# Performance work log

Measured on AMD Instinct MI355X. Metric: run time of the kernel, lower is better.

## Reference

```python
import jax, jax.numpy as jnp
import numpy as np

N_NODES = 50000
N_EDGES = 800000
N_FEAT = 32
DIM_ENC = 64
HEADS = 8
DIM_MLP = 512
NUM_GRAPHS = 2000
NEG_SLOPE = 0.2


def gat_conv(x, edge_index, W, a_src, a_dst, bias, concat):
    """PyG-style GATConv: add self loops, per-head attention, segment softmax over
    incoming edges at the destination node, weighted scatter-sum aggregation."""
    N = x.shape[0]
    H, F = a_src.shape
    h = (x @ W).reshape(N, H, F)                      # [N, H, F]
    loop = jnp.arange(N, dtype=edge_index.dtype)
    src = jnp.concatenate([edge_index[0], loop])      # source j
    dst = jnp.concatenate([edge_index[1], loop])      # target i
    alpha_src = (h * a_src[None]).sum(-1)             # [N, H]
    alpha_dst = (h * a_dst[None]).sum(-1)             # [N, H]
    e = alpha_src[src] + alpha_dst[dst]               # [E', H]
    e = jnp.where(e > 0, e, NEG_SLOPE * e)            # leaky_relu
    # segment softmax over edges sharing the same destination node
    m = jax.ops.segment_max(e, dst, num_segments=N)
    ex = jnp.exp(e - m[dst])
    s = jax.ops.segment_sum(ex, dst, num_segments=N)
    alpha = ex / (s[dst] + 1e-16)                     # [E', H]
    msg = h[src] * alpha[..., None]                   # [E', H, F]
    out = jax.ops.segment_sum(msg, dst, num_segments=N)  # [N, H, F]
    out = out.reshape(N, H * F) if concat else out.mean(axis=1)
    return out + bias


def setup_inputs() -> dict:
    key = jax.random.key(0)
    ks = jax.random.split(key, 16)
    x = jax.random.normal(ks[0], (N_NODES, N_FEAT), dtype=jnp.float32)
    edge_index = jax.random.randint(ks[1], (2, N_EDGES), 0, N_NODES, dtype=jnp.int64)
    batch = jnp.sort(jax.random.randint(ks[2], (N_NODES,), 0, NUM_GRAPHS, dtype=jnp.int64))
    sc = lambda fi, fo: 1.0 / np.sqrt(fi)
    W1 = jax.random.normal(ks[3], (N_FEAT, HEADS * DIM_ENC), dtype=jnp.float32) * sc(N_FEAT, 0)
    a_src1 = jax.random.normal(ks[4], (HEADS, DIM_ENC), dtype=jnp.float32) * sc(DIM_ENC, 0)
    a_dst1 = jax.random.normal(ks[5], (HEADS, DIM_ENC), dtype=jnp.float32) * sc(DIM_ENC, 0)
    b1 = jnp.zeros((DIM_ENC,), dtype=jnp.float32)
    W2 = jax.random.normal(ks[6], (DIM_ENC, HEADS * DIM_ENC), dtype=jnp.float32) * sc(DIM_ENC, 0)
    a_src2 = jax.random.normal(ks[7], (HEADS, DIM_ENC), dtype=jnp.float32) * sc(DIM_ENC, 0)
    a_dst2 = jax.random.normal(ks[8], (HEADS, DIM_ENC), dtype=jnp.float32) * sc(DIM_ENC, 0)
    b2 = jnp.zeros((HEADS * DIM_ENC,), dtype=jnp.float32)
    fcW1 = jax.random.normal(ks[9], (HEADS * DIM_ENC, DIM_MLP), dtype=jnp.float32) * sc(HEADS * DIM_ENC, 0)
    fcb1 = jnp.zeros((DIM_MLP,), dtype=jnp.float32)
    fcW2 = jax.random.normal(ks[10], (DIM_MLP, DIM_MLP), dtype=jnp.float32) * sc(DIM_MLP, 0)
    fcb2 = jnp.zeros((DIM_MLP,), dtype=jnp.float32)
    fcW3 = jax.random.normal(ks[11], (DIM_MLP, 1), dtype=jnp.float32) * sc(DIM_MLP, 0)
    fcb3 = jnp.zeros((1,), dtype=jnp.float32)
    return dict(x=x, edge_index=edge_index, batch=batch,
                W1=W1, a_src1=a_src1, a_dst1=a_dst1, b1=b1,
                W2=W2, a_src2=a_src2, a_dst2=a_dst2, b2=b2,
                fcW1=fcW1, fcb1=fcb1, fcW2=fcW2, fcb2=fcb2, fcW3=fcW3, fcb3=fcb3)


def reference(x, edge_index, batch, W1, a_src1, a_dst1, b1, W2, a_src2, a_dst2, b2,
              fcW1, fcb1, fcW2, fcb2, fcW3, fcb3):
    h = gat_conv(x, edge_index, W1, a_src1, a_dst1, b1, concat=False)   # [N, dim_enc]
    h = gat_conv(h, edge_index, W2, a_src2, a_dst2, b2, concat=True)    # [N, 8*dim_enc]
    g = jax.ops.segment_sum(h, batch, num_segments=NUM_GRAPHS)          # [G, 8*dim_enc]
    g = jax.nn.relu(g @ fcW1 + fcb1)   # dropout is identity in eval / p=0
    g = jax.nn.relu(g @ fcW2 + fcb2)
    return g @ fcW3 + fcb3             # [G, 1]
```

## Files before the change

kernel.cpp:

```cpp
#include <hip/hip_runtime.h>
#include <hip/hip_bf16.h>

#define N_NODES   50000
#define N_EDGES   800000
#define NF        32
#define DE        64
#define NH        8
#define CT        512
#define DMLP      512
#define NG        2000
#define NEGS      0.2f


__global__ void init_count_k(int* __restrict__ cnt) {
    int i = blockIdx.x * 256 + threadIdx.x;
    if (i < N_NODES) cnt[i] = 1;
}

__global__ void hist_k(const int* __restrict__ ei, int* __restrict__ cnt) {
    int e = blockIdx.x * 256 + threadIdx.x;
    if (e < N_EDGES) atomicAdd(&cnt[ei[N_EDGES + e]], 1);
}

__global__ void alloc_off_k(const int* __restrict__ cnt, int* __restrict__ off,
                            int* __restrict__ total) {
    int i = blockIdx.x * 256 + threadIdx.x;
    if (i < N_NODES) off[i] = atomicAdd(total, cnt[i]);
}

__global__ void scatter_k(const int* __restrict__ ei, const int* __restrict__ off,
                          int* __restrict__ cur, int* __restrict__ ssrc) {
    int e = blockIdx.x * 256 + threadIdx.x;
    if (e < N_EDGES) {
        int s = ei[e];
        int d = ei[N_EDGES + e];
        int p = off[d] + atomicAdd(&cur[d], 1);
        ssrc[p] = s;
    } else if (e < N_EDGES + N_NODES) {
        int i = e - N_EDGES;
        int p = off[i] + atomicAdd(&cur[i], 1);
        ssrc[p] = i;
    }
}


__global__ void goffs_k(const int* __restrict__ batch, int* __restrict__ goff) {
    int i = blockIdx.x * 256 + threadIdx.x;
    if (i >= N_NODES) return;
    int b = batch[i];
    if (i == 0) {
        for (int g = 0; g <= b; ++g) goff[g] = 0;
    } else {
        int pb = batch[i - 1];
        for (int g = pb + 1; g <= b; ++g) goff[g] = i;
    }
    if (i == N_NODES - 1) {
        for (int g = b + 1; g <= NG; ++g) goff[g] = N_NODES;
    }
}


__global__ void prep_k(const float* __restrict__ W1, const float* __restrict__ a_s1,
                       const float* __restrict__ a_d1, const float* __restrict__ W2,
                       const float* __restrict__ a_s2, const float* __restrict__ a_d2,
                       float* __restrict__ B1s, float* __restrict__ B1d,
                       float* __restrict__ B2s, float* __restrict__ B2d,
                       float* __restrict__ U1) {
    int idx = blockIdx.x * 256 + threadIdx.x;
    if (idx < 256) {
        int c = idx >> 3, hd = idx & 7;
        float s1 = 0.f, s2 = 0.f;
        for (int f = 0; f < 64; ++f) {
            float w = W1[c * 512 + hd * 64 + f];
            s1 += w * a_s1[hd * 64 + f];
            s2 += w * a_d1[hd * 64 + f];
        }
        B1s[idx] = s1; B1d[idx] = s2;
    } else if (idx < 768) {
        int i2 = idx - 256;
        int c = i2 >> 3, hd = i2 & 7;
        float s1 = 0.f, s2 = 0.f;
        for (int f = 0; f < 64; ++f) {
            float w = W2[c * 512 + hd * 64 + f];
            s1 += w * a_s2[hd * 64 + f];
            s2 += w * a_d2[hd * 64 + f];
        }
        B2s[i2] = s1; B2d[i2] = s2;
    } else if (idx < 768 + 256 * 64) {
        int i2 = idx - 768;
        int k = i2 >> 6, f = i2 & 63;
        int hd = k >> 5, c = k & 31;
        U1[i2] = W1[c * 512 + hd * 64 + f] * 0.125f;
    }
}


template<int C>
__global__ void alpha_x_k(const float* __restrict__ xin, const float* __restrict__ Bs,
                          const float* __restrict__ Bd, float* __restrict__ as_,
                          float* __restrict__ ad_) {
    __shared__ float bs[C * 8], bd[C * 8];
    int tid = threadIdx.x;
    for (int i = tid; i < C * 8; i += 256) { bs[i] = Bs[i]; bd[i] = Bd[i]; }
    __syncthreads();
    int gid = blockIdx.x * 256 + tid;
    if (gid >= N_NODES * NH) return;
    int n = gid >> 3, hd = gid & 7;
    const float4* xp = (const float4*)(xin + (size_t)n * C);
    float s1 = 0.f, s2 = 0.f;
    #pragma unroll
    for (int q = 0; q < C / 4; ++q) {
        float4 v = xp[q];
        int b0 = (q * 4) * 8 + hd;
        s1 += v.x * bs[b0] + v.y * bs[b0 + 8] + v.z * bs[b0 + 16] + v.w * bs[b0 + 24];
        s2 += v.x * bd[b0] + v.y * bd[b0 + 8] + v.z * bd[b0 + 16] + v.w * bd[b0 + 24];
    }
    as_[gid] = s1;
    ad_[gid] = s2;
}


__device__ inline float4 fma4(float a, float4 v, float4 c) {
    c.x = fmaf(a, v.x, c.x); c.y = fmaf(a, v.y, c.y);
    c.z = fmaf(a, v.z, c.z); c.w = fmaf(a, v.w, c.w);
    return c;
}

__device__ inline float edge_w(float e) {
    e = e > 0.f ? e : NEGS * e;
    return __expf(e);
}


__global__ __launch_bounds__(256) void agg1_k(
        const float* __restrict__ x, const float* __restrict__ as_,
        const float* __restrict__ ad_, const int* __restrict__ ssrc,
        const int* __restrict__ off, const int* __restrict__ cnt,
        float* __restrict__ aggx1) {
    int wv = __builtin_amdgcn_readfirstlane(blockIdx.x * 4 + (threadIdx.x >> 6));
    if (wv >= N_NODES) return;
    int lane = threadIdx.x & 63;
    int hd = lane >> 3, q = lane & 7;
    int beg = off[wv], end = beg + cnt[wv];
    float adv = ad_[wv * NH + hd];

    float4 acc = {0.f, 0.f, 0.f, 0.f};
    float wsum = 0.f;
    int j = beg;
    for (; j + 4 <= end; j += 4) {
        int s0 = ssrc[j], s1 = ssrc[j + 1], s2 = ssrc[j + 2], s3 = ssrc[j + 3];
        float e0 = as_[s0 * NH + hd], e1 = as_[s1 * NH + hd];
        float e2 = as_[s2 * NH + hd], e3 = as_[s3 * NH + hd];
        float4 v0 = *(const float4*)(x + s0 * NF + q * 4);
        float4 v1 = *(const float4*)(x + s1 * NF + q * 4);
        float4 v2 = *(const float4*)(x + s2 * NF + q * 4);
        float4 v3 = *(const float4*)(x + s3 * NF + q * 4);
        float w0 = edge_w(e0 + adv), w1 = edge_w(e1 + adv);
        float w2 = edge_w(e2 + adv), w3 = edge_w(e3 + adv);
        wsum += (w0 + w1) + (w2 + w3);
        acc = fma4(w0, v0, acc); acc = fma4(w1, v1, acc);
        acc = fma4(w2, v2, acc); acc = fma4(w3, v3, acc);
    }
    for (; j < end; ++j) {
        int s0 = ssrc[j];
        float w0 = edge_w(as_[s0 * NH + hd] + adv);
        float4 v0 = *(const float4*)(x + s0 * NF + q * 4);
        wsum += w0;
        acc = fma4(w0, v0, acc);
    }
    float inv = 1.f / wsum;
    acc.x *= inv; acc.y *= inv; acc.z *= inv; acc.w *= inv;
    ((float4*)(aggx1 + (size_t)wv * 256))[lane] = acc;
}


template<int K, int N, bool RELU>
__global__ __launch_bounds__(256) void tgemm_k(
        const float* __restrict__ A, const float* __restrict__ W,
        const float* __restrict__ bias, float* __restrict__ Y, int nrows) {
    constexpr int KC = (K < 256) ? K : 256;
    __shared__ float As[KC][64];
    int t = threadIdx.x;
    int row0 = blockIdx.x * 64;
    int col0 = blockIdx.y * 64;
    int rr = t & 63;
    int kb = (t >> 6) * (KC / 4);
    int r0 = (t >> 4) * 4;
    int c0 = (t & 15) * 4;
    float acc[4][4];
    #pragma unroll
    for (int i = 0; i < 4; ++i)
        #pragma unroll
        for (int j = 0; j < 4; ++j) acc[i][j] = 0.f;

    for (int kc = 0; kc < K; kc += KC) {
        if (kc) __syncthreads();
        {
            int grow = row0 + rr;
            const float* ap = A + (size_t)grow * K + kc + kb;
            #pragma unroll
            for (int i = 0; i < KC / 4; i += 4) {
                float4 v = {0.f, 0.f, 0.f, 0.f};
                if (grow < nrows) v = *(const float4*)(ap + i);
                As[kb + i + 0][rr] = v.x;
                As[kb + i + 1][rr] = v.y;
                As[kb + i + 2][rr] = v.z;
                As[kb + i + 3][rr] = v.w;
            }
        }
        __syncthreads();
        const float* wp = W + (size_t)kc * N + col0 + c0;
        #pragma unroll 4
        for (int k = 0; k < KC; ++k) {
            float4 a = *(const float4*)&As[k][r0];
            float4 w = *(const float4*)(wp + (size_t)k * N);
            acc[0][0] = fmaf(a.x, w.x, acc[0][0]); acc[0][1] = fmaf(a.x, w.y, acc[0][1]);
            acc[0][2] = fmaf(a.x, w.z, acc[0][2]); acc[0][3] = fmaf(a.x, w.w, acc[0][3]);
            acc[1][0] = fmaf(a.y, w.x, acc[1][0]); acc[1][1] = fmaf(a.y, w.y, acc[1][1]);
            acc[1][2] = fmaf(a.y, w.z, acc[1][2]); acc[1][3] = fmaf(a.y, w.w, acc[1][3]);
            acc[2][0] = fmaf(a.z, w.x, acc[2][0]); acc[2][1] = fmaf(a.z, w.y, acc[2][1]);
            acc[2][2] = fmaf(a.z, w.z, acc[2][2]); acc[2][3] = fmaf(a.z, w.w, acc[2][3]);
            acc[3][0] = fmaf(a.w, w.x, acc[3][0]); acc[3][1] = fmaf(a.w, w.y, acc[3][1]);
            acc[3][2] = fmaf(a.w, w.z, acc[3][2]); acc[3][3] = fmaf(a.w, w.w, acc[3][3]);
        }
    }
    float4 bv = *(const float4*)(bias + col0 + c0);
    #pragma unroll
    for (int i = 0; i < 4; ++i) {
        int row = row0 + r0 + i;
        if (row < nrows) {
            float4 o;
            o.x = acc[i][0] + bv.x; o.y = acc[i][1] + bv.y;
            o.z = acc[i][2] + bv.z; o.w = acc[i][3] + bv.w;
            if (RELU) {
                o.x = fmaxf(o.x, 0.f); o.y = fmaxf(o.y, 0.f);
                o.z = fmaxf(o.z, 0.f); o.w = fmaxf(o.w, 0.f);
            }
            *(float4*)&Y[(size_t)row * N + col0 + c0] = o;
        }
    }
}


__global__ __launch_bounds__(256) void agg2g_k(
        const float* __restrict__ hx, const float* __restrict__ as_,
        const float* __restrict__ ad_, const int* __restrict__ ssrc,
        const int* __restrict__ off, const int* __restrict__ cnt,
        const int* __restrict__ goff, float* __restrict__ P) {
    int g = blockIdx.x;
    int w = threadIdx.x >> 6;
    int lane = threadIdx.x & 63;
    int hd = lane >> 3, q = lane & 7;
    int nbeg = goff[g], nend = goff[g + 1];

    __shared__ float sp[4][512];

    float4 p0 = {0.f, 0.f, 0.f, 0.f}, p1 = {0.f, 0.f, 0.f, 0.f};

    for (int nd0 = nbeg + w; nd0 < nend; nd0 += 4) {
        int nd = __builtin_amdgcn_readfirstlane(nd0);
        int beg = off[nd], end = beg + cnt[nd];
        float adv = ad_[nd * NH + hd];

        float4 a0 = {0.f, 0.f, 0.f, 0.f}, a1 = {0.f, 0.f, 0.f, 0.f};
        float wsum = 0.f;
        int j = beg;
        for (; j + 4 <= end; j += 4) {
            int s0 = ssrc[j], s1 = ssrc[j + 1], s2 = ssrc[j + 2], s3 = ssrc[j + 3];
            float e0 = as_[s0 * NH + hd], e1 = as_[s1 * NH + hd];
            float e2 = as_[s2 * NH + hd], e3 = as_[s3 * NH + hd];
            const float4* pp0 = (const float4*)(hx + s0 * DE + q * 8);
            const float4* pp1 = (const float4*)(hx + s1 * DE + q * 8);
            const float4* pp2 = (const float4*)(hx + s2 * DE + q * 8);
            const float4* pp3 = (const float4*)(hx + s3 * DE + q * 8);
            float4 v00 = pp0[0], v01 = pp0[1];
            float4 v10 = pp1[0], v11 = pp1[1];
            float4 v20 = pp2[0], v21 = pp2[1];
            float4 v30 = pp3[0], v31 = pp3[1];
            float w0 = edge_w(e0 + adv), w1 = edge_w(e1 + adv);
            float w2 = edge_w(e2 + adv), w3 = edge_w(e3 + adv);
            wsum += (w0 + w1) + (w2 + w3);
            a0 = fma4(w0, v00, a0); a1 = fma4(w0, v01, a1);
            a0 = fma4(w1, v10, a0); a1 = fma4(w1, v11, a1);
            a0 = fma4(w2, v20, a0); a1 = fma4(w2, v21, a1);
            a0 = fma4(w3, v30, a0); a1 = fma4(w3, v31, a1);
        }
        for (; j < end; ++j) {
            int s0 = ssrc[j];
            float w0 = edge_w(as_[s0 * NH + hd] + adv);
            const float4* pp0 = (const float4*)(hx + s0 * DE + q * 8);
            float4 v00 = pp0[0], v01 = pp0[1];
            wsum += w0;
            a0 = fma4(w0, v00, a0); a1 = fma4(w0, v01, a1);
        }
        float inv = 1.f / wsum;
        p0 = fma4(inv, a0, p0);
        p1 = fma4(inv, a1, p1);
    }

    ((float4*)&sp[w][lane * 8])[0] = p0;
    ((float4*)&sp[w][lane * 8 + 4])[0] = p1;
    __syncthreads();
    int t = threadIdx.x;
    float s0 = sp[0][t] + sp[1][t] + sp[2][t] + sp[3][t];
    float s1 = sp[0][t + 256] + sp[1][t + 256] + sp[2][t + 256] + sp[3][t + 256];
    P[(size_t)g * CT + t]       = s0;
    P[(size_t)g * CT + t + 256] = s1;
}


__global__ void proj2_k(const float* __restrict__ P, const float* __restrict__ W2,
                        const float* __restrict__ b2, const int* __restrict__ goff,
                        float* __restrict__ g0) {
    int gid = blockIdx.x * 256 + threadIdx.x;
    if (gid >= NG * CT) return;
    int b = gid >> 9, ch = gid & 511;
    int hd = ch >> 6, f = ch & 63;
    const float* Pp = P + (size_t)b * CT + hd * 64;
    int cnt = goff[b + 1] - goff[b];
    float acc = (float)cnt * b2[ch];
    #pragma unroll 4
    for (int c = 0; c < 64; ++c)
        acc = fmaf(Pp[c], W2[c * 512 + hd * 64 + f], acc);
    g0[gid] = acc;
}

__global__ void mlp_out_k(const float* __restrict__ gin, const float* __restrict__ w,
                          const float* __restrict__ b, float* __restrict__ out) {
    int row = blockIdx.x * 4 + (threadIdx.x >> 6);
    int lane = threadIdx.x & 63;
    if (row >= NG) return;
    float s = 0.f;
    for (int k = lane; k < DMLP; k += 64) s += gin[(size_t)row * DMLP + k] * w[k];
    #pragma unroll
    for (int d = 32; d >= 1; d >>= 1) s += __shfl_xor(s, d, 64);
    if (lane == 0) out[row] = s + b[0];
}


extern "C" void kernel_launch(void* const* d_in, const int* in_sizes, int n_in,
                              void* d_out, int out_size, void* d_ws, size_t ws_size,
                              hipStream_t stream) {
    const float* x     = (const float*)d_in[0];
    const int*   ei    = (const int*)d_in[1];
    const int*   batch = (const int*)d_in[2];
    const float* W1    = (const float*)d_in[3];
    const float* asrc1 = (const float*)d_in[4];
    const float* adst1 = (const float*)d_in[5];
    const float* b1    = (const float*)d_in[6];
    const float* W2    = (const float*)d_in[7];
    const float* asrc2 = (const float*)d_in[8];
    const float* adst2 = (const float*)d_in[9];
    const float* b2    = (const float*)d_in[10];
    const float* fcW1  = (const float*)d_in[11];
    const float* fcb1  = (const float*)d_in[12];
    const float* fcW2  = (const float*)d_in[13];
    const float* fcb2  = (const float*)d_in[14];
    const float* fcW3  = (const float*)d_in[15];
    const float* fcb3  = (const float*)d_in[16];

    char* p = (char*)d_ws;
    auto take = [&](size_t bytes) {
        char* r = p;
        p += (bytes + 255) & ~(size_t)255;
        return r;
    };
    float* aggx1 = (float*)take((size_t)N_NODES * 256 * 4);
    float* hx    = (float*)take((size_t)N_NODES * DE * 4);
    float* as_   = (float*)take((size_t)N_NODES * NH * 4);
    float* ad_   = (float*)take((size_t)N_NODES * NH * 4);
    int*   ssrc  = (int*)take((size_t)(N_EDGES + N_NODES) * 4);
    int*   offv  = (int*)take((size_t)N_NODES * 4);
    int*   cntv  = (int*)take((size_t)N_NODES * 4);
    int*   cur   = (int*)take((size_t)N_NODES * 4);
    int*   total = (int*)take(256);
    int*   goff  = (int*)take((size_t)(NG + 1) * 4);
    float* B1s   = (float*)take(256 * 4);
    float* B1d   = (float*)take(256 * 4);
    float* B2s   = (float*)take(512 * 4);
    float* B2d   = (float*)take(512 * 4);
    float* U1    = (float*)take(256 * 64 * 4);
    float* P     = (float*)take((size_t)NG * CT * 4);
    float* g0    = (float*)take((size_t)NG * DMLP * 4);
    float* g1    = (float*)take((size_t)NG * DMLP * 4);
    float* g2    = (float*)take((size_t)NG * DMLP * 4);

    init_count_k<<<(N_NODES + 255) / 256, 256, 0, stream>>>(cntv);
    hist_k<<<(N_EDGES + 255) / 256, 256, 0, stream>>>(ei, cntv);
    hipMemsetAsync(total, 0, 4, stream);
    hipMemsetAsync(cur, 0, (size_t)N_NODES * 4, stream);
    alloc_off_k<<<(N_NODES + 255) / 256, 256, 0, stream>>>(cntv, offv, total);
    scatter_k<<<(N_EDGES + N_NODES + 255) / 256, 256, 0, stream>>>(ei, offv, cur, ssrc);
    goffs_k<<<(N_NODES + 255) / 256, 256, 0, stream>>>(batch, goff);

    prep_k<<<(768 + 256 * 64 + 255) / 256, 256, 0, stream>>>(
        W1, asrc1, adst1, W2, asrc2, adst2, B1s, B1d, B2s, B2d, U1);

    alpha_x_k<NF><<<(N_NODES * NH + 255) / 256, 256, 0, stream>>>(x, B1s, B1d, as_, ad_);
    agg1_k<<<(N_NODES + 3) / 4, 256, 0, stream>>>(x, as_, ad_, ssrc, offv, cntv, aggx1);
    {
        dim3 grid((N_NODES + 63) / 64, 1);
        tgemm_k<256, 64, false><<<grid, 256, 0, stream>>>(aggx1, U1, b1, hx, N_NODES);
    }

    alpha_x_k<DE><<<(N_NODES * NH + 255) / 256, 256, 0, stream>>>(hx, B2s, B2d, as_, ad_);
    agg2g_k<<<NG, 256, 0, stream>>>(hx, as_, ad_, ssrc, offv, cntv, goff, P);
    proj2_k<<<(NG * CT + 255) / 256, 256, 0, stream>>>(P, W2, b2, goff, g0);

    {
        dim3 grid((NG + 63) / 64, DMLP / 64);
        tgemm_k<DMLP, DMLP, true><<<grid, 256, 0, stream>>>(g0, fcW1, fcb1, g1, NG);
        tgemm_k<DMLP, DMLP, true><<<grid, 256, 0, stream>>>(g1, fcW2, fcb2, g2, NG);
    }
    mlp_out_k<<<(NG + 3) / 4, 256, 0, stream>>>(g2, fcW3, fcb3, (float*)d_out);
}
```

Measured before the change: 409.9 us.

## Merge setup kernels, fuse layer-2 projection into aggregation, deepen agg1 unroll

Folds the count init, memsets, graph-offset build, weight prep and layer-1 attention logits into one multi-role setup kernel, removing several launches. Each block recomputes the small W1·a vectors in shared memory instead of reading a precomputed buffer. The per-graph layer-2 aggregation now runs with 8 waves per block and applies the W2 projection in the same kernel, which drops the P intermediate and the separate projection launch. agg1 unrolls its edge loop to 8 with loads batched ahead to raise memory-level parallelism, at some cost in registers.

Measured after the change: 426.6 us. 4.1% more time.

```diff
diff --git a/kernel.cpp b/kernel.cpp
--- a/kernel.cpp
+++ b/kernel.cpp
@@ -12,10 +12,99 @@
 #define NEGS      0.2f
 
 
-__global__ void init_count_k(int* __restrict__ cnt) {
-    int i = blockIdx.x * 256 + threadIdx.x;
-    if (i < N_NODES) cnt[i] = 1;
-}
+__device__ inline float4 fma4(float a, float4 v, float4 c) {
+    c.x = fmaf(a, v.x, c.x); c.y = fmaf(a, v.y, c.y);
+    c.z = fmaf(a, v.z, c.z); c.w = fmaf(a, v.w, c.w);
+    return c;
+}
+
+__device__ inline float edge_w(float e) {
+    e = e > 0.f ? e : NEGS * e;
+    return __expf(e);
+}
+
+
+#define SB_A 1563
+#define SB_I 196
+#define SB_U 64
+#define SB_G 196
+#define SB_B 2
+
+__global__ __launch_bounds__(256) void setup_k(
+        const float* __restrict__ x, const float* __restrict__ W1,
+        const float* __restrict__ as1, const float* __restrict__ ad1,
+        const float* __restrict__ W2, const float* __restrict__ as2,
+        const float* __restrict__ ad2, const int* __restrict__ batch,
+        int* __restrict__ cnt, int* __restrict__ cur, int* __restrict__ total,
+        float* __restrict__ U1, int* __restrict__ goff,
+        float* __restrict__ B2s, float* __restrict__ B2d,
+        float* __restrict__ as_, float* __restrict__ ad_) {
+    int b = blockIdx.x;
+    int tid = threadIdx.x;
+    if (b < SB_A) {
+        __shared__ float bs[256], bd[256];
+        {
+            int c = tid >> 3, hd = tid & 7;
+            const float* wr = W1 + c * 512 + hd * 64;
+            const float* p1 = as1 + hd * 64;
+            const float* p2 = ad1 + hd * 64;
+            float s1 = 0.f, s2 = 0.f;
+            #pragma unroll 8
+            for (int f = 0; f < 64; ++f) { float w = wr[f]; s1 += w * p1[f]; s2 += w * p2[f]; }
+            bs[tid] = s1; bd[tid] = s2;
+        }
+        __syncthreads();
+        int gid = b * 256 + tid;
+        if (gid < N_NODES * NH) {
+            int n = gid >> 3, hd = gid & 7;
+            const float4* xp = (const float4*)(x + (size_t)n * NF);
+            float s1 = 0.f, s2 = 0.f;
+            #pragma unroll
+            for (int qq = 0; qq < NF / 4; ++qq) {
+                float4 v = xp[qq];
+                int b0 = qq * 32 + hd;
+                s1 += v.x * bs[b0] + v.y * bs[b0 + 8] + v.z * bs[b0 + 16] + v.w * bs[b0 + 24];
+                s2 += v.x * bd[b0] + v.y * bd[b0 + 8] + v.z * bd[b0 + 16] + v.w * bd[b0 + 24];
+            }
+            as_[gid] = s1;
+            ad_[gid] = s2;
+        }
+    } else if (b < SB_A + SB_I) {
+        int i = (b - SB_A) * 256 + tid;
+        if (i < N_NODES) { cnt[i] = 1; cur[i] = 0; }
+        if (i == 0) total[0] = 0;
+    } else if (b < SB_A + SB_I + SB_U) {
+        int i = (b - SB_A - SB_I) * 256 + tid;
+        int k = i >> 6, f = i & 63;
+        int hd = k >> 5, c = k & 31;
+        U1[i] = W1[c * 512 + hd * 64 + f] * 0.125f;
+    } else if (b < SB_A + SB_I + SB_U + SB_G) {
+        int i = (b - SB_A - SB_I - SB_U) * 256 + tid;
+        if (i < N_NODES) {
+            int bb = batch[i];
+            if (i == 0) {
+                for (int g = 0; g <= bb; ++g) goff[g] = 0;
+            } else {
+                int pb = batch[i - 1];
+                for (int g = pb + 1; g <= bb; ++g) goff[g] = i;
+            }
+            if (i == N_NODES - 1) {
+                for (int g = bb + 1; g <= NG; ++g) goff[g] = N_NODES;
+            }
+        }
+    } else {
+        int i = (b - SB_A - SB_I - SB_U - SB_G) * 256 + tid;
+        int c = i >> 3, hd = i & 7;
+        const float* wr = W2 + c * 512 + hd * 64;
+        const float* p1 = as2 + hd * 64;
+        const float* p2 = ad2 + hd * 64;
+        float s1 = 0.f, s2 = 0.f;
+        #pragma unroll 8
+        for (int f = 0; f < 64; ++f) { float w = wr[f]; s1 += w * p1[f]; s2 += w * p2[f]; }
+        B2s[i] = s1; B2d[i] = s2;
+    }
+}
+
 
 __global__ void hist_k(const int* __restrict__ ei, int* __restrict__ cnt) {
     int e = blockIdx.x * 256 + threadIdx.x;
@@ -44,91 +133,27 @@
 }
 
 
-__global__ void goffs_k(const int* __restrict__ batch, int* __restrict__ goff) {
-    int i = blockIdx.x * 256 + threadIdx.x;
-    if (i >= N_NODES) return;
-    int b = batch[i];
-    if (i == 0) {
-        for (int g = 0; g <= b; ++g) goff[g] = 0;
-    } else {
-        int pb = batch[i - 1];
-        for (int g = pb + 1; g <= b; ++g) goff[g] = i;
-    }
-    if (i == N_NODES - 1) {
-        for (int g = b + 1; g <= NG; ++g) goff[g] = N_NODES;
-    }
-}
-
-
-__global__ void prep_k(const float* __restrict__ W1, const float* __restrict__ a_s1,
-                       const float* __restrict__ a_d1, const float* __restrict__ W2,
-                       const float* __restrict__ a_s2, const float* __restrict__ a_d2,
-                       float* __restrict__ B1s, float* __restrict__ B1d,
-                       float* __restrict__ B2s, float* __restrict__ B2d,
-                       float* __restrict__ U1) {
-    int idx = blockIdx.x * 256 + threadIdx.x;
-    if (idx < 256) {
-        int c = idx >> 3, hd = idx & 7;
-        float s1 = 0.f, s2 = 0.f;
-        for (int f = 0; f < 64; ++f) {
-            float w = W1[c * 512 + hd * 64 + f];
-            s1 += w * a_s1[hd * 64 + f];
-            s2 += w * a_d1[hd * 64 + f];
-        }
-        B1s[idx] = s1; B1d[idx] = s2;
-    } else if (idx < 768) {
-        int i2 = idx - 256;
-        int c = i2 >> 3, hd = i2 & 7;
-        float s1 = 0.f, s2 = 0.f;
-        for (int f = 0; f < 64; ++f) {
-            float w = W2[c * 512 + hd * 64 + f];
-            s1 += w * a_s2[hd * 64 + f];
-            s2 += w * a_d2[hd * 64 + f];
-        }
-        B2s[i2] = s1; B2d[i2] = s2;
-    } else if (idx < 768 + 256 * 64) {
-        int i2 = idx - 768;
-        int k = i2 >> 6, f = i2 & 63;
-        int hd = k >> 5, c = k & 31;
-        U1[i2] = W1[c * 512 + hd * 64 + f] * 0.125f;
-    }
-}
-
-
-template<int C>
-__global__ void alpha_x_k(const float* __restrict__ xin, const float* __restrict__ Bs,
-                          const float* __restrict__ Bd, float* __restrict__ as_,
-                          float* __restrict__ ad_) {
-    __shared__ float bs[C * 8], bd[C * 8];
+__global__ void alpha2_k(const float* __restrict__ hx, const float* __restrict__ Bs,
+                         const float* __restrict__ Bd, float* __restrict__ as_,
+                         float* __restrict__ ad_) {
+    __shared__ float bs[512], bd[512];
     int tid = threadIdx.x;
-    for (int i = tid; i < C * 8; i += 256) { bs[i] = Bs[i]; bd[i] = Bd[i]; }
+    for (int i = tid; i < 512; i += 256) { bs[i] = Bs[i]; bd[i] = Bd[i]; }
     __syncthreads();
     int gid = blockIdx.x * 256 + tid;
     if (gid >= N_NODES * NH) return;
     int n = gid >> 3, hd = gid & 7;
-    const float4* xp = (const float4*)(xin + (size_t)n * C);
+    const float4* xp = (const float4*)(hx + (size_t)n * DE);
     float s1 = 0.f, s2 = 0.f;
     #pragma unroll
-    for (int q = 0; q < C / 4; ++q) {
-        float4 v = xp[q];
-        int b0 = (q * 4) * 8 + hd;
+    for (int qq = 0; qq < DE / 4; ++qq) {
+        float4 v = xp[qq];
+        int b0 = qq * 32 + hd;
         s1 += v.x * bs[b0] + v.y * bs[b0 + 8] + v.z * bs[b0 + 16] + v.w * bs[b0 + 24];
         s2 += v.x * bd[b0] + v.y * bd[b0 + 8] + v.z * bd[b0 + 16] + v.w * bd[b0 + 24];
     }
     as_[gid] = s1;
     ad_[gid] = s2;
-}
-
-
-__device__ inline float4 fma4(float a, float4 v, float4 c) {
-    c.x = fmaf(a, v.x, c.x); c.y = fmaf(a, v.y, c.y);
-    c.z = fmaf(a, v.z, c.z); c.w = fmaf(a, v.w, c.w);
-    return c;
-}
-
-__device__ inline float edge_w(float e) {
-    e = e > 0.f ? e : NEGS * e;
-    return __expf(e);
 }
 
 
@@ -147,19 +172,20 @@
     float4 acc = {0.f, 0.f, 0.f, 0.f};
     float wsum = 0.f;
     int j = beg;
-    for (; j + 4 <= end; j += 4) {
-        int s0 = ssrc[j], s1 = ssrc[j + 1], s2 = ssrc[j + 2], s3 = ssrc[j + 3];
-        float e0 = as_[s0 * NH + hd], e1 = as_[s1 * NH + hd];
-        float e2 = as_[s2 * NH + hd], e3 = as_[s3 * NH + hd];
-        float4 v0 = *(const float4*)(x + s0 * NF + q * 4);
-        float4 v1 = *(const float4*)(x + s1 * NF + q * 4);
-        float4 v2 = *(const float4*)(x + s2 * NF + q * 4);
-        float4 v3 = *(const float4*)(x + s3 * NF + q * 4);
-        float w0 = edge_w(e0 + adv), w1 = edge_w(e1 + adv);
-        float w2 = edge_w(e2 + adv), w3 = edge_w(e3 + adv);
-        wsum += (w0 + w1) + (w2 + w3);
-        acc = fma4(w0, v0, acc); acc = fma4(w1, v1, acc);
-        acc = fma4(w2, v2, acc); acc = fma4(w3, v3, acc);
+    for (; j + 8 <= end; j += 8) {
+        int s[8]; float ev[8]; float4 v[8];
+        #pragma unroll
+        for (int u = 0; u < 8; ++u) s[u] = ssrc[j + u];
+        #pragma unroll
+        for (int u = 0; u < 8; ++u) ev[u] = as_[s[u] * NH + hd];
+        #pragma unroll
+        for (int u = 0; u < 8; ++u) v[u] = *(const float4*)(x + s[u] * NF + q * 4);
+        #pragma unroll
+        for (int u = 0; u < 8; ++u) {
+            float w = edge_w(ev[u] + adv);
+            wsum += w;
+            acc = fma4(w, v[u], acc);
+        }
     }
     for (; j < end; ++j) {
         int s0 = ssrc[j];
@@ -242,22 +268,24 @@
 }
 
 
-__global__ __launch_bounds__(256) void agg2g_k(
+__global__ __launch_bounds__(512) void agg2gp_k(
         const float* __restrict__ hx, const float* __restrict__ as_,
         const float* __restrict__ ad_, const int* __restrict__ ssrc,
         const int* __restrict__ off, const int* __restrict__ cnt,
-        const int* __restrict__ goff, float* __restrict__ P) {
+        const int* __restrict__ goff, const float* __restrict__ W2,
+        const float* __restrict__ b2, float* __restrict__ g0) {
     int g = blockIdx.x;
     int w = threadIdx.x >> 6;
     int lane = threadIdx.x & 63;
     int hd = lane >> 3, q = lane & 7;
     int nbeg = goff[g], nend = goff[g + 1];
 
-    __shared__ float sp[4][512];
+    __shared__ float sp[8][512];
+    __shared__ float ps[512];
 
     float4 p0 = {0.f, 0.f, 0.f, 0.f}, p1 = {0.f, 0.f, 0.f, 0.f};
 
-    for (int nd0 = nbeg + w; nd0 < nend; nd0 += 4) {
+    for (int nd0 = nbeg + w; nd0 < nend; nd0 += 8) {
         int nd = __builtin_amdgcn_readfirstlane(nd0);
         int beg = off[nd], end = beg + cnt[nd];
         float adv = ad_[nd * NH + hd];
@@ -298,32 +326,29 @@
         p1 = fma4(inv, a1, p1);
     }
 
-    ((float4*)&sp[w][lane * 8])[0] = p0;
-    ((float4*)&sp[w][lane * 8 + 4])[0] = p1;
+    *(float4*)&sp[w][lane * 8]     = p0;
+    *(float4*)&sp[w][lane * 8 + 4] = p1;
     __syncthreads();
     int t = threadIdx.x;
-    float s0 = sp[0][t] + sp[1][t] + sp[2][t] + sp[3][t];
-    float s1 = sp[0][t + 256] + sp[1][t + 256] + sp[2][t + 256] + sp[3][t + 256];
-    P[(size_t)g * CT + t]       = s0;
-    P[(size_t)g * CT + t + 256] = s1;
-}
-
-
-__global__ void proj2_k(const float* __restrict__ P, const float* __restrict__ W2,
-                        const float* __restrict__ b2, const int* __restrict__ goff,
-                        float* __restrict__ g0) {
-    int gid = blockIdx.x * 256 + threadIdx.x;
-    if (gid >= NG * CT) return;
-    int b = gid >> 9, ch = gid & 511;
-    int hd = ch >> 6, f = ch & 63;
-    const float* Pp = P + (size_t)b * CT + hd * 64;
-    int cnt = goff[b + 1] - goff[b];
-    float acc = (float)cnt * b2[ch];
-    #pragma unroll 4
+    {
+        float s = 0.f;
+        #pragma unroll
+        for (int ww = 0; ww < 8; ++ww) s += sp[ww][t];
+        ps[t] = s;
+    }
+    __syncthreads();
+
+    int hd2 = t >> 6, f = t & 63;
+    int cn = nend - nbeg;
+    float acc = (float)cn * b2[t];
+    const float* pp = &ps[hd2 * 64];
+    const float* wp = W2 + hd2 * 64 + f;
+    #pragma unroll 8
     for (int c = 0; c < 64; ++c)
-        acc = fmaf(Pp[c], W2[c * 512 + hd * 64 + f], acc);
-    g0[gid] = acc;
-}
+        acc = fmaf(pp[c], wp[(size_t)c * 512], acc);
+    g0[(size_t)g * CT + t] = acc;
+}
+
 
 __global__ void mlp_out_k(const float* __restrict__ gin, const float* __restrict__ w,
                           const float* __restrict__ b, float* __restrict__ out) {
@@ -375,37 +400,29 @@
     int*   cur   = (int*)take((size_t)N_NODES * 4);
     int*   total = (int*)take(256);
     int*   goff  = (int*)take((size_t)(NG + 1) * 4);
-    float* B1s   = (float*)take(256 * 4);
-    float* B1d   = (float*)take(256 * 4);
     float* B2s   = (float*)take(512 * 4);
     float* B2d   = (float*)take(512 * 4);
     float* U1    = (float*)take(256 * 64 * 4);
-    float* P     = (float*)take((size_t)NG * CT * 4);
     float* g0    = (float*)take((size_t)NG * DMLP * 4);
     float* g1    = (float*)take((size_t)NG * DMLP * 4);
     float* g2    = (float*)take((size_t)NG * DMLP * 4);
 
-    init_count_k<<<(N_NODES + 255) / 256, 256, 0, stream>>>(cntv);
+    setup_k<<<SB_A + SB_I + SB_U + SB_G + SB_B, 256, 0, stream>>>(
+        x, W1, asrc1, adst1, W2, asrc2, adst2, batch,
+        cntv, cur, total, U1, goff, B2s, B2d, as_, ad_);
+
     hist_k<<<(N_EDGES + 255) / 256, 256, 0, stream>>>(ei, cntv);
-    hipMemsetAsync(total, 0, 4, stream);
-    hipMemsetAsync(cur, 0, (size_t)N_NODES * 4, stream);
     alloc_off_k<<<(N_NODES + 255) / 256, 256, 0, stream>>>(cntv, offv, total);
     scatter_k<<<(N_EDGES + N_NODES + 255) / 256, 256, 0, stream>>>(ei, offv, cur, ssrc);
-    goffs_k<<<(N_NODES + 255) / 256, 256, 0, stream>>>(batch, goff);
-
-    prep_k<<<(768 + 256 * 64 + 255) / 256, 256, 0, stream>>>(
-        W1, asrc1, adst1, W2, asrc2, adst2, B1s, B1d, B2s, B2d, U1);
-
-    alpha_x_k<NF><<<(N_NODES * NH + 255) / 256, 256, 0, stream>>>(x, B1s, B1d, as_, ad_);
+
     agg1_k<<<(N_NODES + 3) / 4, 256, 0, stream>>>(x, as_, ad_, ssrc, offv, cntv, aggx1);
     {
         dim3 grid((N_NODES + 63) / 64, 1);
         tgemm_k<256, 64, false><<<grid, 256, 0, stream>>>(aggx1, U1, b1, hx, N_NODES);
     }
 
-    alpha_x_k<DE><<<(N_NODES * NH + 255) / 256, 256, 0, stream>>>(hx, B2s, B2d, as_, ad_);
-    agg2g_k<<<NG, 256, 0, stream>>>(hx, as_, ad_, ssrc, offv, cntv, goff, P);
-    proj2_k<<<(NG * CT + 255) / 256, 256, 0, stream>>>(P, W2, b2, goff, g0);
+    alpha2_k<<<(N_NODES * NH + 255) / 256, 256, 0, stream>>>(hx, B2s, B2d, as_, ad_);
+    agg2gp_k<<<NG, 512, 0, stream>>>(hx, as_, ad_, ssrc, offv, cntv, goff, W2, b2, g0);
 
     {
         dim3 grid((NG + 63) / 64, DMLP / 64);
```
